# Optimization experiments

Measured on AMD Instinct MI355X. Metric: run time of the kernel, lower is better.

The kernel has to match this reference:

```python
import jax, jax.numpy as jnp
import numpy as np


def setup_inputs() -> dict:
    key = jax.random.key(0)
    k1, k2 = jax.random.split(key)
    x = jax.random.normal(k1, (32, 256, 56, 56), dtype=jnp.float32)
    # Conv2d(2 -> 1, kernel 7x7, bias=False): weight [out_c=1, in_c=2, 7, 7]
    w_conv = jax.random.normal(k2, (1, 2, 7, 7), dtype=jnp.float32) * 0.1
    return {"x": x, "w_conv": w_conv}


def reference(x, w_conv):
    # channel-wise average and max pooling -> [B, 2, H, W]
    avgout = jnp.mean(x, axis=1, keepdims=True)
    maxout = jnp.max(x, axis=1, keepdims=True)
    x1 = jnp.concatenate([avgout, maxout], axis=1)
    # 7x7 conv, padding=3 (SAME), NCHW / OIHW
    x1 = jax.lax.conv_general_dilated(
        x1, w_conv,
        window_strides=(1, 1),
        padding=((3, 3), (3, 3)),
        dimension_numbers=("NCHW", "OIHW", "NCHW"),
    )
    gate = jax.nn.sigmoid(x1)  # [B, 1, H, W]
    return x * gate
```

## Files before the change

### kernel.cpp

```cpp
#include <hip/hip_runtime.h>
#include <math.h>

#define B_    32
#define C_    256
#define H_    56
#define W_    56
#define HW_   (H_ * W_)
#define BHW_  (B_ * HW_)
#define HW4_  (HW_ / 4)
#define NF4_  (BHW_ / 4)
#define GRID_ 512
#define F4PB_ (NF4_ / GRID_)
#define POSPB_ (BHW_ / GRID_)

typedef float f4v __attribute__((ext_vector_type(4)));

__global__ __launch_bounds__(256) void sa_reduce_kernel(
    const float* __restrict__ x, float* __restrict__ pool) {
  const int t = threadIdx.x;
  const int lane = t & 31;
  const int cgrp = t >> 5;
  const f4v* __restrict__ x4 = (const f4v*)x;
  f4v* __restrict__ p4 = (f4v*)pool;

  __shared__ f4v ssum[8][32];
  __shared__ f4v smax[8][32];

#pragma unroll
  for (int sub = 0; sub < 2; ++sub) {
    const int lidx = sub * 32 + lane;
    const bool active = (lidx < F4PB_);
    const unsigned if4 = (unsigned)blockIdx.x * F4PB_ + (active ? lidx : 0);
    const unsigned bimg = if4 / HW4_;
    const unsigned hw4 = if4 % HW4_;
    const unsigned base = (bimg * C_ + cgrp) * HW4_ + hw4;

    f4v s = {0.f, 0.f, 0.f, 0.f};
    f4v m = {-INFINITY, -INFINITY, -INFINITY, -INFINITY};
#pragma unroll 8
    for (int k = 0; k < 32; ++k) {
      f4v v = x4[base + (unsigned)(k * 8) * HW4_];
      s += v;
      m = (f4v){fmaxf(m.x, v.x), fmaxf(m.y, v.y),
                fmaxf(m.z, v.z), fmaxf(m.w, v.w)};
    }
    ssum[cgrp][lane] = s;
    smax[cgrp][lane] = m;
    __syncthreads();
    if (t < 32 && sub * 32 + t < F4PB_) {
      f4v S = ssum[0][t];
      f4v M = smax[0][t];
#pragma unroll
      for (int g = 1; g < 8; ++g) {
        f4v sg = ssum[g][t];
        f4v mg = smax[g][t];
        S += sg;
        M = (f4v){fmaxf(M.x, mg.x), fmaxf(M.y, mg.y),
                  fmaxf(M.z, mg.z), fmaxf(M.w, mg.w)};
      }
      const unsigned jf4 = (unsigned)blockIdx.x * F4PB_ + sub * 32 + t;
      const unsigned bb = jf4 / HW4_;
      const unsigned hh = jf4 % HW4_;
      p4[bb * 2 * HW4_ + hh]        = S * (1.0f / (float)C_);
      p4[bb * 2 * HW4_ + HW4_ + hh] = M;
    }
    __syncthreads();
  }
}

__global__ __launch_bounds__(256) void sa_conv_apply_kernel(
    const float* __restrict__ x, const float* __restrict__ pool,
    const float* __restrict__ wt, float* __restrict__ out) {
  const int t = threadIdx.x;
  __shared__ f4v sgate4[F4PB_];

  if (t < POSPB_) {
    const unsigned p = (unsigned)blockIdx.x * POSPB_ + (unsigned)t;
    const unsigned bimg = p / HW_;
    const unsigned hw = p % HW_;
    const int h = (int)(hw / W_);
    const int w = (int)(hw % W_);
    const float* pl0 = pool + (long)bimg * 2 * HW_;
    float acc = 0.f;
#pragma unroll
    for (int ic = 0; ic < 2; ++ic) {
      const float* pl = pl0 + ic * HW_;
      const float* wr0 = wt + ic * 49;
#pragma unroll
      for (int kh = 0; kh < 7; ++kh) {
        const int ih = h + kh - 3;
        if (ih < 0 || ih >= H_) continue;
        const float* row = pl + ih * W_;
        const float* wr = wr0 + kh * 7;
#pragma unroll
        for (int kw = 0; kw < 7; ++kw) {
          const int iw = w + kw - 3;
          if (iw < 0 || iw >= W_) continue;
          acc = fmaf(row[iw], wr[kw], acc);
        }
      }
    }
    ((float*)sgate4)[t] = 1.0f / (1.0f + __expf(-acc));
  }
  __syncthreads();

  const int lane = t & 31;
  const int cgrp = t >> 5;
  const f4v* __restrict__ x4 = (const f4v*)x;
  f4v* __restrict__ o4 = (f4v*)out;
#pragma unroll
  for (int sub = 0; sub < 2; ++sub) {
    const int lidx = sub * 32 + lane;
    if (lidx >= F4PB_) continue;
    const unsigned if4 = (unsigned)blockIdx.x * F4PB_ + lidx;
    const unsigned bimg = if4 / HW4_;
    const unsigned hw4 = if4 % HW4_;
    const unsigned base = (bimg * C_ + cgrp) * HW4_ + hw4;
    const f4v g = sgate4[lidx];
#pragma unroll 8
    for (int k = 0; k < 32; ++k) {
      const unsigned idx = base + (unsigned)(k * 8) * HW4_;
      f4v v = x4[idx];
      __builtin_nontemporal_store(v * g, &o4[idx]);
    }
  }
}

extern "C" void kernel_launch(void* const* d_in, const int* in_sizes, int n_in,
                              void* d_out, int out_size, void* d_ws, size_t ws_size,
                              hipStream_t stream) {
  const float* x  = (const float*)d_in[0];
  const float* wc = (const float*)d_in[1];
  float* out = (float*)d_out;
  float* pool = (float*)d_ws;

  sa_reduce_kernel<<<GRID_, 256, 0, stream>>>(x, pool);
  sa_conv_apply_kernel<<<GRID_, 256, 0, stream>>>(x, pool, wc, out);
}
```

Before: 218.3 us.

## Retile both kernels to 16-float4 chunks over 1568 blocks and split conv channels

Increases the grid to 1568 blocks, each handling 16 float4 positions across 16 channel groups of 16 channels, which removes the idle second sub-pass caused by the 49-wide chunk. The conv gate computation is split so that two threads per position each handle one input channel, and the results are summed through shared memory. This aims for better occupancy and latency hiding on the bandwidth-bound passes, at the cost of shorter contiguous segments per wavefront and an extra barrier.

New measurement: 204.7 us. 6.2% less time.

```diff
diff --git a/kernel.cpp b/kernel.cpp
--- a/kernel.cpp
+++ b/kernel.cpp
@@ -9,62 +9,56 @@
 #define BHW_  (B_ * HW_)
 #define HW4_  (HW_ / 4)
 #define NF4_  (BHW_ / 4)
-#define GRID_ 512
-#define F4PB_ (NF4_ / GRID_)
-#define POSPB_ (BHW_ / GRID_)
+#define GRID_ 1568
+#define CHUNKF4_ (NF4_ / GRID_)
+#define POSPB_  (BHW_ / GRID_)
 
 typedef float f4v __attribute__((ext_vector_type(4)));
 
 __global__ __launch_bounds__(256) void sa_reduce_kernel(
     const float* __restrict__ x, float* __restrict__ pool) {
   const int t = threadIdx.x;
-  const int lane = t & 31;
-  const int cgrp = t >> 5;
+  const int lane = t & 15;
+  const int cgrp = t >> 4;
+  const unsigned if4 = (unsigned)blockIdx.x * CHUNKF4_ + lane;
+  const unsigned bimg = if4 / HW4_;
+  const unsigned hw4 = if4 % HW4_;
   const f4v* __restrict__ x4 = (const f4v*)x;
-  f4v* __restrict__ p4 = (f4v*)pool;
+  const unsigned base = (bimg * C_ + cgrp) * HW4_ + hw4;
 
-  __shared__ f4v ssum[8][32];
-  __shared__ f4v smax[8][32];
+  f4v s = {0.f, 0.f, 0.f, 0.f};
+  f4v m = {-INFINITY, -INFINITY, -INFINITY, -INFINITY};
+#pragma unroll 8
+  for (int k = 0; k < 16; ++k) {
+    f4v v = x4[base + (unsigned)(k * 16) * HW4_];
+    s += v;
+    m = (f4v){fmaxf(m.x, v.x), fmaxf(m.y, v.y),
+              fmaxf(m.z, v.z), fmaxf(m.w, v.w)};
+  }
 
+  __shared__ f4v ssum[16][16];
+  __shared__ f4v smax[16][16];
+  ssum[cgrp][lane] = s;
+  smax[cgrp][lane] = m;
+  __syncthreads();
+
+  if (t < 16) {
+    f4v S = ssum[0][t];
+    f4v M = smax[0][t];
 #pragma unroll
-  for (int sub = 0; sub < 2; ++sub) {
-    const int lidx = sub * 32 + lane;
-    const bool active = (lidx < F4PB_);
-    const unsigned if4 = (unsigned)blockIdx.x * F4PB_ + (active ? lidx : 0);
-    const unsigned bimg = if4 / HW4_;
-    const unsigned hw4 = if4 % HW4_;
-    const unsigned base = (bimg * C_ + cgrp) * HW4_ + hw4;
-
-    f4v s = {0.f, 0.f, 0.f, 0.f};
-    f4v m = {-INFINITY, -INFINITY, -INFINITY, -INFINITY};
-#pragma unroll 8
-    for (int k = 0; k < 32; ++k) {
-      f4v v = x4[base + (unsigned)(k * 8) * HW4_];
-      s += v;
-      m = (f4v){fmaxf(m.x, v.x), fmaxf(m.y, v.y),
-                fmaxf(m.z, v.z), fmaxf(m.w, v.w)};
+    for (int g = 1; g < 16; ++g) {
+      f4v sg = ssum[g][t];
+      f4v mg = smax[g][t];
+      S += sg;
+      M = (f4v){fmaxf(M.x, mg.x), fmaxf(M.y, mg.y),
+                fmaxf(M.z, mg.z), fmaxf(M.w, mg.w)};
     }
-    ssum[cgrp][lane] = s;
-    smax[cgrp][lane] = m;
-    __syncthreads();
-    if (t < 32 && sub * 32 + t < F4PB_) {
-      f4v S = ssum[0][t];
-      f4v M = smax[0][t];
-#pragma unroll
-      for (int g = 1; g < 8; ++g) {
-        f4v sg = ssum[g][t];
-        f4v mg = smax[g][t];
-        S += sg;
-        M = (f4v){fmaxf(M.x, mg.x), fmaxf(M.y, mg.y),
-                  fmaxf(M.z, mg.z), fmaxf(M.w, mg.w)};
-      }
-      const unsigned jf4 = (unsigned)blockIdx.x * F4PB_ + sub * 32 + t;
-      const unsigned bb = jf4 / HW4_;
-      const unsigned hh = jf4 % HW4_;
-      p4[bb * 2 * HW4_ + hh]        = S * (1.0f / (float)C_);
-      p4[bb * 2 * HW4_ + HW4_ + hh] = M;
-    }
-    __syncthreads();
+    f4v* p4 = (f4v*)pool;
+    const unsigned jf4 = (unsigned)blockIdx.x * CHUNKF4_ + t;
+    const unsigned bb = jf4 / HW4_;
+    const unsigned hh = jf4 % HW4_;
+    p4[bb * 2 * HW4_ + hh]        = S * (1.0f / (float)C_);
+    p4[bb * 2 * HW4_ + HW4_ + hh] = M;
   }
 }
 
@@ -72,57 +66,56 @@
     const float* __restrict__ x, const float* __restrict__ pool,
     const float* __restrict__ wt, float* __restrict__ out) {
   const int t = threadIdx.x;
-  __shared__ f4v sgate4[F4PB_];
+  __shared__ float partial[128];
+  __shared__ f4v sgate4[CHUNKF4_];
 
-  if (t < POSPB_) {
-    const unsigned p = (unsigned)blockIdx.x * POSPB_ + (unsigned)t;
+  if (t < 2 * POSPB_) {
+    const int pos = t >> 1;
+    const int ic = t & 1;
+    const unsigned p = (unsigned)blockIdx.x * POSPB_ + (unsigned)pos;
     const unsigned bimg = p / HW_;
     const unsigned hw = p % HW_;
     const int h = (int)(hw / W_);
     const int w = (int)(hw % W_);
-    const float* pl0 = pool + (long)bimg * 2 * HW_;
+    const float* pl = pool + ((long)bimg * 2 + ic) * HW_;
+    const float* wr0 = wt + ic * 49;
     float acc = 0.f;
 #pragma unroll
-    for (int ic = 0; ic < 2; ++ic) {
-      const float* pl = pl0 + ic * HW_;
-      const float* wr0 = wt + ic * 49;
+    for (int kh = 0; kh < 7; ++kh) {
+      const int ih = h + kh - 3;
+      if (ih < 0 || ih >= H_) continue;
+      const float* row = pl + ih * W_;
+      const float* wr = wr0 + kh * 7;
 #pragma unroll
-      for (int kh = 0; kh < 7; ++kh) {
-        const int ih = h + kh - 3;
-        if (ih < 0 || ih >= H_) continue;
-        const float* row = pl + ih * W_;
-        const float* wr = wr0 + kh * 7;
-#pragma unroll
-        for (int kw = 0; kw < 7; ++kw) {
-          const int iw = w + kw - 3;
-          if (iw < 0 || iw >= W_) continue;
-          acc = fmaf(row[iw], wr[kw], acc);
-        }
+      for (int kw = 0; kw < 7; ++kw) {
+        const int iw = w + kw - 3;
+        if (iw < 0 || iw >= W_) continue;
+        acc = fmaf(row[iw], wr[kw], acc);
       }
     }
-    ((float*)sgate4)[t] = 1.0f / (1.0f + __expf(-acc));
+    partial[t] = acc;
+  }
+  __syncthreads();
+  if (t < POSPB_) {
+    float a = partial[2 * t] + partial[2 * t + 1];
+    ((float*)sgate4)[t] = 1.0f / (1.0f + __expf(-a));
   }
   __syncthreads();
 
-  const int lane = t & 31;
-  const int cgrp = t >> 5;
+  const int lane = t & 15;
+  const int cgrp = t >> 4;
+  const unsigned if4 = (unsigned)blockIdx.x * CHUNKF4_ + lane;
+  const unsigned bimg = if4 / HW4_;
+  const unsigned hw4 = if4 % HW4_;
+  const unsigned base = (bimg * C_ + cgrp) * HW4_ + hw4;
   const f4v* __restrict__ x4 = (const f4v*)x;
   f4v* __restrict__ o4 = (f4v*)out;
-#pragma unroll
-  for (int sub = 0; sub < 2; ++sub) {
-    const int lidx = sub * 32 + lane;
-    if (lidx >= F4PB_) continue;
-    const unsigned if4 = (unsigned)blockIdx.x * F4PB_ + lidx;
-    const unsigned bimg = if4 / HW4_;
-    const unsigned hw4 = if4 % HW4_;
-    const unsigned base = (bimg * C_ + cgrp) * HW4_ + hw4;
-    const f4v g = sgate4[lidx];
+  const f4v g = sgate4[lane];
 #pragma unroll 8
-    for (int k = 0; k < 32; ++k) {
-      const unsigned idx = base + (unsigned)(k * 8) * HW4_;
-      f4v v = x4[idx];
-      __builtin_nontemporal_store(v * g, &o4[idx]);
-    }
+  for (int k = 0; k < 16; ++k) {
+    const unsigned idx = base + (unsigned)(k * 16) * HW4_;
+    f4v v = x4[idx];
+    __builtin_nontemporal_store(v * g, &o4[idx]);
   }
 }
 
```
